# Kernel tuning notes

Measured on AMD Instinct MI355X. Metric: run time of the kernel, lower is better.

Reference implementation:

```python
import jax, jax.numpy as jnp
import numpy as np

N = 50000
E = 800000
IN, H1, H2, OUT = 128, 256, 256, 128


def gcn_conv(x, edge_index, W, b):
    """PyG GCNConv with normalize=True, add_self_loops=True.
    out = D^-1/2 (A + I) D^-1/2 (x @ W) + b, messages flow src->dst."""
    n = x.shape[0]
    h = x @ W  # [N, C_out]
    src, dst = edge_index[0], edge_index[1]
    # degree of (A + I) at each destination node (all edge weights = 1)
    deg = jax.ops.segment_sum(jnp.ones(src.shape[0], dtype=x.dtype), dst, num_segments=n) + 1.0
    dinv = jax.lax.rsqrt(deg)  # deg >= 1, safe
    norm = dinv[src] * dinv[dst]  # [E]
    agg = jax.ops.segment_sum(h[src] * norm[:, None], dst, num_segments=n)
    # self-loop contribution: norm_ii = dinv[i]^2
    return agg + h * (dinv * dinv)[:, None] + b


def setup_inputs() -> dict:
    key = jax.random.key(0)
    ks = jax.random.split(key, 12)
    node_feature = jax.random.normal(ks[0], (N, IN), dtype=jnp.float32)
    edge_index = jax.random.randint(ks[1], (2, E), 0, N, dtype=jnp.int64)
    edge_index_new = jax.random.randint(ks[2], (2, E), 0, N, dtype=jnp.int64)
    def glorot(k, fan_in, fan_out):
        s = jnp.sqrt(6.0 / (fan_in + fan_out)).astype(jnp.float32)
        return jax.random.uniform(k, (fan_in, fan_out), jnp.float32, -s, s)
    return {
        "node_feature": node_feature,
        "edge_index": edge_index,
        "edge_index_new": edge_index_new,
        "W0": glorot(ks[3], IN, H1), "b0": jnp.zeros((H1,), jnp.float32),
        "W1": glorot(ks[4], IN, H2), "b1": jnp.zeros((H2,), jnp.float32),
        "W2": glorot(ks[5], H1, OUT), "b2": jnp.zeros((OUT,), jnp.float32),
        "W3": glorot(ks[6], H2, OUT), "b3": jnp.zeros((OUT,), jnp.float32),
    }


def reference(node_feature, edge_index, edge_index_new, W0, b0, W1, b1, W2, b2, W3, b3):
    tmp1 = jax.nn.relu(gcn_conv(node_feature, edge_index, W0, b0))
    tmp2 = jax.nn.relu(gcn_conv(node_feature, edge_index_new, W1, b1))
    out1 = gcn_conv(tmp1, edge_index, W2, b2)
    out2 = gcn_conv(tmp2, edge_index_new, W3, b3)
    return out1 + out2
```

## Files before the change

kernel.cpp:

```cpp
#include <hip/hip_runtime.h>


typedef unsigned int uint;
typedef unsigned short ushort;
typedef __attribute__((ext_vector_type(8))) short bf8_t;
typedef __attribute__((ext_vector_type(4))) float f4_t;

#define CHUNK 4096
#define MAXNB 800

__device__ inline ushort f2bf(float f) {
    uint u = __float_as_uint(f);
    return (ushort)((u + 0x7fff + ((u >> 16) & 1)) >> 16);
}
__device__ inline float bf2f(ushort h) { return __uint_as_float(((uint)h) << 16); }

__global__ __launch_bounds__(256) void k_p1_hist(
    const int* __restrict__ ei_a, const int* __restrict__ ei_b,
    int* __restrict__ cnt_mat, int e, int NB, int NW) {
    __shared__ int lh[MAXNB];
    int l = blockIdx.x / NW, w = blockIdx.x % NW;
    const int* dst = (l ? ei_b : ei_a) + e;
    for (int t = threadIdx.x; t < NB; t += 256) lh[t] = 0;
    __syncthreads();
    int beg = w * CHUNK, end = min(beg + CHUNK, e);
    for (int j = beg + threadIdx.x; j < end; j += 256) atomicAdd(&lh[dst[j] >> 6], 1);
    __syncthreads();
    int* outp = cnt_mat + ((size_t)l * NW + w) * NB;
    for (int t = threadIdx.x; t < NB; t += 256) outp[t] = lh[t];
}

__global__ __launch_bounds__(256) void k_p2a(const int* __restrict__ cnt_mat,
                                             int* __restrict__ wgoff, int* __restrict__ btot,
                                             int NB, int NW) {
    __shared__ int s[256];
    int which = blockIdx.x;
    int l = which / NB, b = which - l * NB;
    int t = threadIdx.x;
    int v = (t < NW) ? cnt_mat[((size_t)l * NW + t) * NB + b] : 0;
    s[t] = v;
    __syncthreads();
    for (int o = 1; o < 256; o <<= 1) {
        int x = 0;
        if (t >= o) x = s[t - o];
        __syncthreads();
        s[t] += x;
        __syncthreads();
    }
    if (t < NW) wgoff[((size_t)l * NB + b) * NW + t] = s[t] - v;
    if (t == 255) btot[which] = s[255];
}

__global__ __launch_bounds__(256) void k_p2b(const int* __restrict__ btot,
                                             int* __restrict__ boff, int NB, int e) {
    __shared__ int s[1024];
    for (int l = 0; l < 2; ++l) {
        for (int t = threadIdx.x; t < 1024; t += 256) s[t] = (t < NB) ? btot[l * NB + t] : 0;
        __syncthreads();
        for (int o = 1; o < 1024; o <<= 1) {
            int tmp[4];
#pragma unroll
            for (int k = 0; k < 4; ++k) {
                int idx = threadIdx.x + k * 256;
                tmp[k] = (idx >= o) ? s[idx - o] : 0;
            }
            __syncthreads();
#pragma unroll
            for (int k = 0; k < 4; ++k) s[threadIdx.x + k * 256] += tmp[k];
            __syncthreads();
        }
        for (int t = threadIdx.x; t < NB; t += 256)
            boff[l * (NB + 1) + t] = s[t] - btot[l * NB + t];
        if (threadIdx.x == 0) boff[l * (NB + 1) + NB] = e;
        __syncthreads();
    }
}

__global__ __launch_bounds__(256) void k_p3_scatter(
    const int* __restrict__ ei_a, const int* __restrict__ ei_b,
    const int* __restrict__ wgoff, const int* __restrict__ boff,
    int* __restrict__ ebuf_a, int* __restrict__ ebuf_b, int e, int NB, int NW) {
    __shared__ int base[MAXNB];
    __shared__ int bump[MAXNB];
    int l = blockIdx.x / NW, w = blockIdx.x % NW;
    const int* ei = l ? ei_b : ei_a;
    int* ebuf = l ? ebuf_b : ebuf_a;
    for (int t = threadIdx.x; t < NB; t += 256) {
        base[t] = boff[l * (NB + 1) + t] + wgoff[((size_t)l * NB + t) * NW + w];
        bump[t] = 0;
    }
    __syncthreads();
    int beg = w * CHUNK, end = min(beg + CHUNK, e);
    for (int j = beg + threadIdx.x; j < end; j += 256) {
        int sv = ei[j], d = ei[e + j];
        int b = d >> 6;
        int pos = base[b] + atomicAdd(&bump[b], 1);
        ebuf[pos] = ((d & 63) << 17) | sv;
    }
}

__global__ __launch_bounds__(256) void k_p4_nodesort(
    const int* __restrict__ ebuf_a, const int* __restrict__ ebuf_b,
    const int* __restrict__ boff, int* __restrict__ csr_a, int* __restrict__ csr_b,
    int* __restrict__ noff, float* __restrict__ dinv, int n, int e, int NB) {
    __shared__ int hist[64], nstart[64];
    int which = blockIdx.x;
    int l = which / NB, b = which - l * NB;
    const int* ebuf = l ? ebuf_b : ebuf_a;
    int* csr = l ? csr_b : csr_a;
    int seg0 = boff[l * (NB + 1) + b], seg1 = boff[l * (NB + 1) + b + 1];
    if (threadIdx.x < 64) hist[threadIdx.x] = 0;
    __syncthreads();
    for (int j = seg0 + (int)threadIdx.x; j < seg1; j += 256)
        atomicAdd(&hist[ebuf[j] >> 17], 1);
    __syncthreads();
    if (threadIdx.x < 64) {
        int v = hist[threadIdx.x];
        int s = v;
#pragma unroll
        for (int o = 1; o < 64; o <<= 1) {
            int t = __shfl_up(s, o, 64);
            if ((int)threadIdx.x >= o) s += t;
        }
        int node = b * 64 + (int)threadIdx.x;
        nstart[threadIdx.x] = seg0 + s - v;
        if (node < n) {
            noff[(size_t)l * (n + 1) + node] = seg0 + s - v;
            dinv[(size_t)l * n + node] = rsqrtf((float)v + 1.0f);
        }
        hist[threadIdx.x] = 0;
    }
    if (b == NB - 1 && threadIdx.x == 0) noff[(size_t)l * (n + 1) + n] = e;
    __syncthreads();
    for (int j = seg0 + (int)threadIdx.x; j < seg1; j += 256) {
        int pk = ebuf[j];
        int ni = pk >> 17;
        int pos = nstart[ni] + atomicAdd(&hist[ni], 1);
        csr[pos] = pk & 0x1ffff;
    }
}

__global__ void k_cvt(const float2* __restrict__ x2, const float* __restrict__ dinv,
                      uint* __restrict__ xba, uint* __restrict__ xbb, int n) {
    int i = blockIdx.x * blockDim.x + threadIdx.x;
    if (i >= n * 64) return;
    int node = i >> 6;
    float da = dinv[node], db = dinv[n + node];
    float2 v = x2[i];
    xba[i] = (uint)f2bf(da * v.x) | ((uint)f2bf(da * v.y) << 16);
    xbb[i] = (uint)f2bf(db * v.x) | ((uint)f2bf(db * v.y) << 16);
}

__global__ void k_pack_all(const float* __restrict__ W0, const float* __restrict__ W1,
                           const float* __restrict__ W2, const float* __restrict__ W3,
                           ushort* __restrict__ Wpb) {
    int i = blockIdx.x * blockDim.x + threadIdx.x;
    if (i >= 4 * 32768) return;
    int seg = i >> 15;
    int r = i & 32767;
    const float* W = seg == 0 ? W0 : seg == 1 ? W1 : seg == 2 ? W2 : W3;
    int N = seg < 2 ? 256 : 128;
    int k = r / N, nn = r - k * N;
    int kt = k >> 5, q = (k & 31) >> 3, jj = k & 7;
    int nt = nn >> 4, ln = q * 16 + (nn & 15);
    int NT = N >> 4;
    Wpb[(size_t)seg * 32768 + (((size_t)(kt * NT + nt)) * 64 + ln) * 8 + jj] = f2bf(W[r]);
}

__device__ inline void gather_row(const uint* __restrict__ xb, const int* __restrict__ ep,
                                  int m, int lane, float& ax, float& ay) {
    int j = 0;
    for (; j + 8 <= m; j += 8) {
        int4 s4 = *(const int4*)(ep + j);
        int4 s5 = *(const int4*)(ep + j + 4);
        uint u0 = xb[(size_t)s4.x * 64 + lane];
        uint u1 = xb[(size_t)s4.y * 64 + lane];
        uint u2 = xb[(size_t)s4.z * 64 + lane];
        uint u3 = xb[(size_t)s4.w * 64 + lane];
        uint u4 = xb[(size_t)s5.x * 64 + lane];
        uint u5 = xb[(size_t)s5.y * 64 + lane];
        uint u6 = xb[(size_t)s5.z * 64 + lane];
        uint u7 = xb[(size_t)s5.w * 64 + lane];
        ax += bf2f((ushort)u0) + bf2f((ushort)u1) + bf2f((ushort)u2) + bf2f((ushort)u3) +
              bf2f((ushort)u4) + bf2f((ushort)u5) + bf2f((ushort)u6) + bf2f((ushort)u7);
        ay += bf2f((ushort)(u0 >> 16)) + bf2f((ushort)(u1 >> 16)) +
              bf2f((ushort)(u2 >> 16)) + bf2f((ushort)(u3 >> 16)) +
              bf2f((ushort)(u4 >> 16)) + bf2f((ushort)(u5 >> 16)) +
              bf2f((ushort)(u6 >> 16)) + bf2f((ushort)(u7 >> 16));
    }
    for (; j + 4 <= m; j += 4) {
        int4 s4 = *(const int4*)(ep + j);
        uint u0 = xb[(size_t)s4.x * 64 + lane];
        uint u1 = xb[(size_t)s4.y * 64 + lane];
        uint u2 = xb[(size_t)s4.z * 64 + lane];
        uint u3 = xb[(size_t)s4.w * 64 + lane];
        ax += bf2f((ushort)u0) + bf2f((ushort)u1) + bf2f((ushort)u2) + bf2f((ushort)u3);
        ay += bf2f((ushort)(u0 >> 16)) + bf2f((ushort)(u1 >> 16)) +
              bf2f((ushort)(u2 >> 16)) + bf2f((ushort)(u3 >> 16));
    }
    for (; j < m; ++j) {
        uint u = xb[(size_t)ep[j] * 64 + lane];
        ax += bf2f((ushort)u);
        ay += bf2f((ushort)(u >> 16));
    }
}

__global__ __launch_bounds__(256) void k_gather_l1(
    const uint* __restrict__ xba, const uint* __restrict__ xbb,
    const int* __restrict__ csr_a, const int* __restrict__ csr_b,
    const int* __restrict__ noff, const float* __restrict__ dinv,
    uint* __restrict__ ta, uint* __restrict__ tb, int n, int gb) {
    int bid = blockIdx.x;
    int br = bid >= gb;
    const uint* xb = br ? xbb : xba;
    const int* csr = br ? csr_b : csr_a;
    const int* no = noff + (size_t)br * (n + 1);
    const float* dv = dinv + (size_t)br * n;
    uint* outp = br ? tb : ta;
    int node = ((bid - (br ? gb : 0)) * 256 + (int)threadIdx.x) >> 6;
    if (node >= n) return;
    node = __builtin_amdgcn_readfirstlane(node);
    const int lane = threadIdx.x & 63;
    int beg = no[node], m = no[node + 1] - beg;
    uint us = xb[(size_t)node * 64 + lane];
    float ax = 0.f, ay = 0.f;
    gather_row(xb, csr + beg, m, lane, ax, ay);
    float di = dv[node];
    uint o = (uint)f2bf(di * (ax + bf2f((ushort)us))) |
             ((uint)f2bf(di * (ay + bf2f((ushort)(us >> 16)))) << 16);
    outp[(size_t)node * 64 + lane] = o;
}

__global__ __launch_bounds__(256) void k_gather_l2(
    const uint* __restrict__ hba, const uint* __restrict__ hbb,
    const int* __restrict__ csr_a, const int* __restrict__ csr_b,
    const int* __restrict__ noff, const float* __restrict__ dinv,
    const float* __restrict__ b2, const float* __restrict__ b3,
    float* __restrict__ out, int n) {
    int node = (blockIdx.x * 256 + (int)threadIdx.x) >> 6;
    if (node >= n) return;
    node = __builtin_amdgcn_readfirstlane(node);
    const int lane = threadIdx.x & 63;

    int beg = noff[node], m = noff[node + 1] - beg;
    float ax = 0.f, ay = 0.f;
    gather_row(hba, csr_a + beg, m, lane, ax, ay);
    uint usa = hba[(size_t)node * 64 + lane];
    float da = dinv[node];
    float vx = da * (ax + bf2f((ushort)usa));
    float vy = da * (ay + bf2f((ushort)(usa >> 16)));

    const int* no_b = noff + (n + 1);
    int beg2 = no_b[node], m2 = no_b[node + 1] - beg2;
    float bx = 0.f, by = 0.f;
    gather_row(hbb, csr_b + beg2, m2, lane, bx, by);
    uint usb = hbb[(size_t)node * 64 + lane];
    float db = dinv[n + node];
    vx += db * (bx + bf2f((ushort)usb));
    vy += db * (by + bf2f((ushort)(usb >> 16)));

    const int f = lane * 2;
    float2 o;
    o.x = b2[f] + b3[f] + vx;
    o.y = b2[f + 1] + b3[f + 1] + vy;
    *(float2*)(out + (size_t)node * 128 + f) = o;
}

__global__ __launch_bounds__(256) void k_mlp_fused(
    const ushort* __restrict__ ta, const ushort* __restrict__ tb,
    const ushort* __restrict__ Wpb, const float* __restrict__ b0,
    const float* __restrict__ b1, const float* __restrict__ dinv,
    ushort* __restrict__ oa, ushort* __restrict__ ob, int n) {
    constexpr int LDW = 264;
    __shared__ ushort hs[64 * LDW];
    const int br = blockIdx.y;
    const ushort* Ap  = br ? tb : ta;
    const ushort* W1  = Wpb + (br ? 32768 : 0);
    const ushort* W2  = Wpb + (br ? 3 * 32768 : 2 * 32768);
    const float* bias = br ? b1 : b0;
    const float* dv   = dinv + (br ? n : 0);
    ushort* Cout      = br ? ob : oa;

    const int lane = threadIdx.x & 63;
    const int wave = threadIdx.x >> 6;
    const int l15 = lane & 15;
    const int quad = lane >> 4;
    const int row_blk = blockIdx.x * 64;

    {
        f4_t acc[4][4];
#pragma unroll
        for (int a = 0; a < 4; ++a)
#pragma unroll
            for (int b = 0; b < 4; ++b) acc[a][b] = (f4_t){0.f, 0.f, 0.f, 0.f};

#pragma unroll
        for (int kt = 0; kt < 4; ++kt) {
            bf8_t af[4];
#pragma unroll
            for (int mi = 0; mi < 4; ++mi) {
                int row = row_blk + mi * 16 + l15;
                if (row < n)
                    af[mi] = *(const bf8_t*)(Ap + (size_t)row * 128 + kt * 32 + quad * 8);
                else
                    af[mi] = (bf8_t){0, 0, 0, 0, 0, 0, 0, 0};
            }
#pragma unroll
            for (int nj = 0; nj < 4; ++nj) {
                int nt = wave * 4 + nj;
                bf8_t wf = *(const bf8_t*)(W1 + (((size_t)(kt * 16 + nt)) * 64 + lane) * 8);
#pragma unroll
                for (int mi = 0; mi < 4; ++mi)
                    acc[mi][nj] = __builtin_amdgcn_mfma_f32_16x16x32_bf16(af[mi], wf, acc[mi][nj], 0, 0, 0);
            }
        }
#pragma unroll
        for (int nj = 0; nj < 4; ++nj) {
            int col = wave * 64 + nj * 16 + l15;
            float bv = bias[col];
#pragma unroll
            for (int mi = 0; mi < 4; ++mi)
#pragma unroll
                for (int r = 0; r < 4; ++r) {
                    int rl = mi * 16 + quad * 4 + r;
                    hs[rl * LDW + col] = f2bf(fmaxf(acc[mi][nj][r] + bv, 0.f));
                }
        }
    }
    __syncthreads();

    {
        f4_t acc2[4][2];
#pragma unroll
        for (int a = 0; a < 4; ++a)
#pragma unroll
            for (int b = 0; b < 2; ++b) acc2[a][b] = (f4_t){0.f, 0.f, 0.f, 0.f};

#pragma unroll
        for (int kt = 0; kt < 8; ++kt) {
            bf8_t af[4];
#pragma unroll
            for (int mi = 0; mi < 4; ++mi)
                af[mi] = *(const bf8_t*)&hs[(mi * 16 + l15) * LDW + kt * 32 + quad * 8];
#pragma unroll
            for (int nj = 0; nj < 2; ++nj) {
                int nt = wave * 2 + nj;
                bf8_t wf = *(const bf8_t*)(W2 + (((size_t)(kt * 8 + nt)) * 64 + lane) * 8);
#pragma unroll
                for (int mi = 0; mi < 4; ++mi)
                    acc2[mi][nj] = __builtin_amdgcn_mfma_f32_16x16x32_bf16(af[mi], wf, acc2[mi][nj], 0, 0, 0);
            }
        }
#pragma unroll
        for (int nj = 0; nj < 2; ++nj) {
            int col = wave * 32 + nj * 16 + l15;
#pragma unroll
            for (int mi = 0; mi < 4; ++mi)
#pragma unroll
                for (int r = 0; r < 4; ++r) {
                    int row = row_blk + mi * 16 + quad * 4 + r;
                    if (row < n)
                        Cout[(size_t)row * 128 + col] = f2bf(acc2[mi][nj][r] * dv[row]);
                }
        }
    }
}

extern "C" void kernel_launch(void* const* d_in, const int* in_sizes, int n_in,
                              void* d_out, int out_size, void* d_ws, size_t ws_size,
                              hipStream_t stream) {
    const float* x    = (const float*)d_in[0];
    const int*   ei_a = (const int*)d_in[1];
    const int*   ei_b = (const int*)d_in[2];
    const float* W0 = (const float*)d_in[3];
    const float* b0 = (const float*)d_in[4];
    const float* W1 = (const float*)d_in[5];
    const float* b1 = (const float*)d_in[6];
    const float* W2 = (const float*)d_in[7];
    const float* b2 = (const float*)d_in[8];
    const float* W3 = (const float*)d_in[9];
    const float* b3 = (const float*)d_in[10];
    float* out = (float*)d_out;

    const int n = in_sizes[0] / 128;
    const int e = in_sizes[1] / 2;
    const int NB = (n + 63) / 64;
    const int NW = (e + CHUNK - 1) / CHUNK;

    float*  ws    = (float*)d_ws;
    float*  dinv  = ws;
    uint*   ta    = (uint*)(ws + 2 * (size_t)n);
    uint*   tb    = ta + 64 * (size_t)n;
    uint*   xba   = tb + 64 * (size_t)n;
    uint*   xbb   = xba + 64 * (size_t)n;
    uint*   oa    = xbb + 64 * (size_t)n;
    uint*   ob    = oa + 64 * (size_t)n;
    ushort* Wpb   = (ushort*)(ob + 64 * (size_t)n);
    int* cnt_mat  = (int*)(Wpb + 4 * 32768);
    int* wgoff    = cnt_mat + 2 * (size_t)NW * NB;
    int* btot     = wgoff + 2 * (size_t)NB * NW;
    int* boff     = btot + 2 * NB;
    int* noff     = boff + 2 * (NB + 1);
    int* ebuf_a   = noff + 2 * (n + 1);
    int* ebuf_b   = ebuf_a + e;
    int* csr_a    = ebuf_b + e;
    int* csr_b    = csr_a + e;

    const int B = 256;

    k_p1_hist<<<2 * NW, B, 0, stream>>>(ei_a, ei_b, cnt_mat, e, NB, NW);
    k_p2a<<<2 * NB, B, 0, stream>>>(cnt_mat, wgoff, btot, NB, NW);
    k_p2b<<<1, B, 0, stream>>>(btot, boff, NB, e);
    k_p3_scatter<<<2 * NW, B, 0, stream>>>(ei_a, ei_b, wgoff, boff, ebuf_a, ebuf_b, e, NB, NW);
    k_p4_nodesort<<<2 * NB, B, 0, stream>>>(ebuf_a, ebuf_b, boff, csr_a, csr_b, noff, dinv,
                                            n, e, NB);

    k_cvt<<<(n * 64 + B - 1) / B, B, 0, stream>>>((const float2*)x, dinv, xba, xbb, n);
    k_pack_all<<<(4 * 32768 + B - 1) / B, B, 0, stream>>>(W0, W1, W2, W3, Wpb);

    const int gb = (n + 3) / 4;
    const int mblocks = (n + 63) / 64;

    k_gather_l1<<<2 * gb, B, 0, stream>>>(xba, xbb, csr_a, csr_b, noff, dinv, ta, tb, n, gb);

    k_mlp_fused<<<dim3(mblocks, 2), B, 0, stream>>>((const ushort*)ta, (const ushort*)tb,
                                                    Wpb, b0, b1, dinv,
                                                    (ushort*)oa, (ushort*)ob, n);

    k_gather_l2<<<gb, B, 0, stream>>>(oa, ob, csr_a, csr_b, noff, dinv, b2, b3, out, n);
}
```

Baseline: 314.5 us.

## Fuse layer-1 gather into MLP kernel, widen sort buckets, merge cvt/pack

Layer-1 neighbour aggregation now writes its 32-row tile straight into swizzled shared memory, and the two-layer MFMA MLP consumes it in the same kernel. This removes the global round trip of the aggregated intermediate and one launch. The edge sort now uses 256-node buckets instead of 64, so there are fewer buckets and less scan and scatter overhead, and the cvt and weight-pack kernels are merged into one launch. The trade-offs are a smaller MLP tile with lower MFMA reuse per block and gather latency now in the MLP's critical path. The 256-bucket sort also assumes NB is at most 256, which holds for n=50000.

```diff
diff --git a/kernel.cpp b/kernel.cpp
--- a/kernel.cpp
+++ b/kernel.cpp
@@ -7,7 +7,7 @@
 typedef __attribute__((ext_vector_type(4))) float f4_t;
 
 #define CHUNK 4096
-#define MAXNB 800
+#define BKT 256
 
 __device__ inline ushort f2bf(float f) {
     uint u = __float_as_uint(f);
@@ -18,16 +18,16 @@
 __global__ __launch_bounds__(256) void k_p1_hist(
     const int* __restrict__ ei_a, const int* __restrict__ ei_b,
     int* __restrict__ cnt_mat, int e, int NB, int NW) {
-    __shared__ int lh[MAXNB];
+    __shared__ int lh[BKT];
     int l = blockIdx.x / NW, w = blockIdx.x % NW;
     const int* dst = (l ? ei_b : ei_a) + e;
-    for (int t = threadIdx.x; t < NB; t += 256) lh[t] = 0;
+    if (threadIdx.x < NB) lh[threadIdx.x] = 0;
     __syncthreads();
     int beg = w * CHUNK, end = min(beg + CHUNK, e);
-    for (int j = beg + threadIdx.x; j < end; j += 256) atomicAdd(&lh[dst[j] >> 6], 1);
+    for (int j = beg + threadIdx.x; j < end; j += 256) atomicAdd(&lh[dst[j] >> 8], 1);
     __syncthreads();
     int* outp = cnt_mat + ((size_t)l * NW + w) * NB;
-    for (int t = threadIdx.x; t < NB; t += 256) outp[t] = lh[t];
+    if (threadIdx.x < NB) outp[threadIdx.x] = lh[threadIdx.x];
 }
 
 __global__ __launch_bounds__(256) void k_p2a(const int* __restrict__ cnt_mat,
@@ -53,25 +53,21 @@
 
 __global__ __launch_bounds__(256) void k_p2b(const int* __restrict__ btot,
                                              int* __restrict__ boff, int NB, int e) {
-    __shared__ int s[1024];
+    __shared__ int s[256];
     for (int l = 0; l < 2; ++l) {
-        for (int t = threadIdx.x; t < 1024; t += 256) s[t] = (t < NB) ? btot[l * NB + t] : 0;
-        __syncthreads();
-        for (int o = 1; o < 1024; o <<= 1) {
-            int tmp[4];
-#pragma unroll
-            for (int k = 0; k < 4; ++k) {
-                int idx = threadIdx.x + k * 256;
-                tmp[k] = (idx >= o) ? s[idx - o] : 0;
-            }
+        int t = threadIdx.x;
+        int v = (t < NB) ? btot[l * NB + t] : 0;
+        s[t] = v;
+        __syncthreads();
+        for (int o = 1; o < 256; o <<= 1) {
+            int x = 0;
+            if (t >= o) x = s[t - o];
             __syncthreads();
-#pragma unroll
-            for (int k = 0; k < 4; ++k) s[threadIdx.x + k * 256] += tmp[k];
+            s[t] += x;
             __syncthreads();
         }
-        for (int t = threadIdx.x; t < NB; t += 256)
-            boff[l * (NB + 1) + t] = s[t] - btot[l * NB + t];
-        if (threadIdx.x == 0) boff[l * (NB + 1) + NB] = e;
+        if (t < NB) boff[l * (NB + 1) + t] = s[t] - v;
+        if (t == 0) boff[l * (NB + 1) + NB] = e;
         __syncthreads();
     }
 }
@@ -80,22 +76,23 @@
     const int* __restrict__ ei_a, const int* __restrict__ ei_b,
     const int* __restrict__ wgoff, const int* __restrict__ boff,
     int* __restrict__ ebuf_a, int* __restrict__ ebuf_b, int e, int NB, int NW) {
-    __shared__ int base[MAXNB];
-    __shared__ int bump[MAXNB];
+    __shared__ int base[BKT];
+    __shared__ int bump[BKT];
     int l = blockIdx.x / NW, w = blockIdx.x % NW;
     const int* ei = l ? ei_b : ei_a;
     int* ebuf = l ? ebuf_b : ebuf_a;
-    for (int t = threadIdx.x; t < NB; t += 256) {
-        base[t] = boff[l * (NB + 1) + t] + wgoff[((size_t)l * NB + t) * NW + w];
-        bump[t] = 0;
+    if (threadIdx.x < NB) {
+        base[threadIdx.x] = boff[l * (NB + 1) + threadIdx.x] +
+                            wgoff[((size_t)l * NB + threadIdx.x) * NW + w];
+        bump[threadIdx.x] = 0;
     }
     __syncthreads();
     int beg = w * CHUNK, end = min(beg + CHUNK, e);
     for (int j = beg + threadIdx.x; j < end; j += 256) {
         int sv = ei[j], d = ei[e + j];
-        int b = d >> 6;
+        int b = d >> 8;
         int pos = base[b] + atomicAdd(&bump[b], 1);
-        ebuf[pos] = ((d & 63) << 17) | sv;
+        ebuf[pos] = ((d & 255) << 17) | sv;
     }
 }
 
@@ -103,36 +100,37 @@
     const int* __restrict__ ebuf_a, const int* __restrict__ ebuf_b,
     const int* __restrict__ boff, int* __restrict__ csr_a, int* __restrict__ csr_b,
     int* __restrict__ noff, float* __restrict__ dinv, int n, int e, int NB) {
-    __shared__ int hist[64], nstart[64];
+    __shared__ int hist[256], nstart[256], sc[256];
     int which = blockIdx.x;
     int l = which / NB, b = which - l * NB;
     const int* ebuf = l ? ebuf_b : ebuf_a;
     int* csr = l ? csr_b : csr_a;
     int seg0 = boff[l * (NB + 1) + b], seg1 = boff[l * (NB + 1) + b + 1];
-    if (threadIdx.x < 64) hist[threadIdx.x] = 0;
-    __syncthreads();
-    for (int j = seg0 + (int)threadIdx.x; j < seg1; j += 256)
-        atomicAdd(&hist[ebuf[j] >> 17], 1);
-    __syncthreads();
-    if (threadIdx.x < 64) {
-        int v = hist[threadIdx.x];
-        int s = v;
-#pragma unroll
-        for (int o = 1; o < 64; o <<= 1) {
-            int t = __shfl_up(s, o, 64);
-            if ((int)threadIdx.x >= o) s += t;
-        }
-        int node = b * 64 + (int)threadIdx.x;
-        nstart[threadIdx.x] = seg0 + s - v;
-        if (node < n) {
-            noff[(size_t)l * (n + 1) + node] = seg0 + s - v;
-            dinv[(size_t)l * n + node] = rsqrtf((float)v + 1.0f);
-        }
-        hist[threadIdx.x] = 0;
-    }
-    if (b == NB - 1 && threadIdx.x == 0) noff[(size_t)l * (n + 1) + n] = e;
-    __syncthreads();
-    for (int j = seg0 + (int)threadIdx.x; j < seg1; j += 256) {
+    int t = threadIdx.x;
+    hist[t] = 0;
+    __syncthreads();
+    for (int j = seg0 + t; j < seg1; j += 256) atomicAdd(&hist[ebuf[j] >> 17], 1);
+    __syncthreads();
+    int v = hist[t];
+    sc[t] = v;
+    __syncthreads();
+    for (int o = 1; o < 256; o <<= 1) {
+        int x = 0;
+        if (t >= o) x = sc[t - o];
+        __syncthreads();
+        sc[t] += x;
+        __syncthreads();
+    }
+    nstart[t] = seg0 + sc[t] - v;
+    int node = b * BKT + t;
+    if (node < n) {
+        noff[(size_t)l * (n + 1) + node] = nstart[t];
+        dinv[(size_t)l * n + node] = rsqrtf((float)v + 1.0f);
+    }
+    hist[t] = 0;
+    if (b == NB - 1 && t == 0) noff[(size_t)l * (n + 1) + n] = e;
+    __syncthreads();
+    for (int j = seg0 + t; j < seg1; j += 256) {
         int pk = ebuf[j];
         int ni = pk >> 17;
         int pos = nstart[ni] + atomicAdd(&hist[ni], 1);
@@ -140,31 +138,32 @@
     }
 }
 
-__global__ void k_cvt(const float2* __restrict__ x2, const float* __restrict__ dinv,
-                      uint* __restrict__ xba, uint* __restrict__ xbb, int n) {
-    int i = blockIdx.x * blockDim.x + threadIdx.x;
-    if (i >= n * 64) return;
-    int node = i >> 6;
-    float da = dinv[node], db = dinv[n + node];
-    float2 v = x2[i];
-    xba[i] = (uint)f2bf(da * v.x) | ((uint)f2bf(da * v.y) << 16);
-    xbb[i] = (uint)f2bf(db * v.x) | ((uint)f2bf(db * v.y) << 16);
-}
-
-__global__ void k_pack_all(const float* __restrict__ W0, const float* __restrict__ W1,
+__global__ void k_cvt_pack(const float2* __restrict__ x2, const float* __restrict__ dinv,
+                           uint* __restrict__ xba, uint* __restrict__ xbb,
+                           const float* __restrict__ W0, const float* __restrict__ W1,
                            const float* __restrict__ W2, const float* __restrict__ W3,
-                           ushort* __restrict__ Wpb) {
-    int i = blockIdx.x * blockDim.x + threadIdx.x;
-    if (i >= 4 * 32768) return;
-    int seg = i >> 15;
-    int r = i & 32767;
-    const float* W = seg == 0 ? W0 : seg == 1 ? W1 : seg == 2 ? W2 : W3;
-    int N = seg < 2 ? 256 : 128;
-    int k = r / N, nn = r - k * N;
-    int kt = k >> 5, q = (k & 31) >> 3, jj = k & 7;
-    int nt = nn >> 4, ln = q * 16 + (nn & 15);
-    int NT = N >> 4;
-    Wpb[(size_t)seg * 32768 + (((size_t)(kt * NT + nt)) * 64 + ln) * 8 + jj] = f2bf(W[r]);
+                           ushort* __restrict__ Wpb, int n, int cvtb) {
+    if ((int)blockIdx.x < cvtb) {
+        int i = blockIdx.x * 256 + threadIdx.x;
+        if (i >= n * 64) return;
+        int node = i >> 6;
+        float da = dinv[node], db = dinv[n + node];
+        float2 v = x2[i];
+        xba[i] = (uint)f2bf(da * v.x) | ((uint)f2bf(da * v.y) << 16);
+        xbb[i] = (uint)f2bf(db * v.x) | ((uint)f2bf(db * v.y) << 16);
+    } else {
+        int i = (blockIdx.x - cvtb) * 256 + threadIdx.x;
+        if (i >= 4 * 32768) return;
+        int seg = i >> 15;
+        int r = i & 32767;
+        const float* W = seg == 0 ? W0 : seg == 1 ? W1 : seg == 2 ? W2 : W3;
+        int N = seg < 2 ? 256 : 128;
+        int k = r / N, nn = r - k * N;
+        int kt = k >> 5, q = (k & 31) >> 3, jj = k & 7;
+        int nt = nn >> 4, ln = q * 16 + (nn & 15);
+        int NT = N >> 4;
+        Wpb[(size_t)seg * 32768 + (((size_t)(kt * NT + nt)) * 64 + ln) * 8 + jj] = f2bf(W[r]);
+    }
 }
 
 __device__ inline void gather_row(const uint* __restrict__ xb, const int* __restrict__ ep,
@@ -205,30 +204,127 @@
     }
 }
 
-__global__ __launch_bounds__(256) void k_gather_l1(
+__global__ __launch_bounds__(256) void k_gather_mlp(
     const uint* __restrict__ xba, const uint* __restrict__ xbb,
     const int* __restrict__ csr_a, const int* __restrict__ csr_b,
     const int* __restrict__ noff, const float* __restrict__ dinv,
-    uint* __restrict__ ta, uint* __restrict__ tb, int n, int gb) {
+    const ushort* __restrict__ Wpb, const float* __restrict__ b0,
+    const float* __restrict__ b1, ushort* __restrict__ oa, ushort* __restrict__ ob,
+    int n, int nblk) {
+    constexpr int HW = 264;
+    __shared__ uint As32[32 * 64];
+    __shared__ ushort hs[32 * HW];
+
     int bid = blockIdx.x;
-    int br = bid >= gb;
+    int br = bid >= nblk;
+    int blk = br ? bid - nblk : bid;
     const uint* xb = br ? xbb : xba;
     const int* csr = br ? csr_b : csr_a;
     const int* no = noff + (size_t)br * (n + 1);
     const float* dv = dinv + (size_t)br * n;
-    uint* outp = br ? tb : ta;
-    int node = ((bid - (br ? gb : 0)) * 256 + (int)threadIdx.x) >> 6;
-    if (node >= n) return;
-    node = __builtin_amdgcn_readfirstlane(node);
+    const ushort* W1 = Wpb + (br ? 32768 : 0);
+    const ushort* W2 = Wpb + (br ? 3 * 32768 : 2 * 32768);
+    const float* bias = br ? b1 : b0;
+    ushort* Cout = br ? ob : oa;
+
     const int lane = threadIdx.x & 63;
-    int beg = no[node], m = no[node + 1] - beg;
-    uint us = xb[(size_t)node * 64 + lane];
-    float ax = 0.f, ay = 0.f;
-    gather_row(xb, csr + beg, m, lane, ax, ay);
-    float di = dv[node];
-    uint o = (uint)f2bf(di * (ax + bf2f((ushort)us))) |
-             ((uint)f2bf(di * (ay + bf2f((ushort)(us >> 16)))) << 16);
-    outp[(size_t)node * 64 + lane] = o;
+    const int wave = threadIdx.x >> 6;
+    const int l15 = lane & 15;
+    const int quad = lane >> 4;
+    const int row0 = blk * 32;
+
+    for (int k = 0; k < 8; ++k) {
+        int r = wave * 8 + k;
+        int node = row0 + r;
+        uint o = 0;
+        if (node < n) {
+            node = __builtin_amdgcn_readfirstlane(node);
+            int beg = no[node], m = no[node + 1] - beg;
+            float ax = 0.f, ay = 0.f;
+            gather_row(xb, csr + beg, m, lane, ax, ay);
+            uint us = xb[(size_t)node * 64 + lane];
+            float di = dv[node];
+            o = (uint)f2bf(di * (ax + bf2f((ushort)us))) |
+                ((uint)f2bf(di * (ay + bf2f((ushort)(us >> 16)))) << 16);
+        }
+        int dw = ((((lane >> 2) + r) & 15) << 2) | (lane & 3);
+        As32[r * 64 + dw] = o;
+    }
+    __syncthreads();
+
+    {
+        f4_t acc[2][4];
+#pragma unroll
+        for (int a = 0; a < 2; ++a)
+#pragma unroll
+            for (int b = 0; b < 4; ++b) acc[a][b] = (f4_t){0.f, 0.f, 0.f, 0.f};
+
+#pragma unroll
+        for (int kt = 0; kt < 4; ++kt) {
+            bf8_t af[2];
+#pragma unroll
+            for (int mi = 0; mi < 2; ++mi) {
+                int rr = mi * 16 + l15;
+                int blk16 = (kt * 4 + quad + rr) & 15;
+                af[mi] = *(const bf8_t*)&As32[rr * 64 + blk16 * 4];
+            }
+#pragma unroll
+            for (int nj = 0; nj < 4; ++nj) {
+                int nt = wave * 4 + nj;
+                bf8_t wf = *(const bf8_t*)(W1 + (((size_t)(kt * 16 + nt)) * 64 + lane) * 8);
+#pragma unroll
+                for (int mi = 0; mi < 2; ++mi)
+                    acc[mi][nj] = __builtin_amdgcn_mfma_f32_16x16x32_bf16(af[mi], wf, acc[mi][nj], 0, 0, 0);
+            }
+        }
+#pragma unroll
+        for (int nj = 0; nj < 4; ++nj) {
+            int col = wave * 64 + nj * 16 + l15;
+            float bv = bias[col];
+#pragma unroll
+            for (int mi = 0; mi < 2; ++mi)
+#pragma unroll
+                for (int r = 0; r < 4; ++r)
+                    hs[(mi * 16 + quad * 4 + r) * HW + col] = f2bf(fmaxf(acc[mi][nj][r] + bv, 0.f));
+        }
+    }
+    __syncthreads();
+
+    {
+        f4_t acc2[2][2];
+#pragma unroll
+        for (int a = 0; a < 2; ++a)
+#pragma unroll
+            for (int b = 0; b < 2; ++b) acc2[a][b] = (f4_t){0.f, 0.f, 0.f, 0.f};
+
+#pragma unroll
+        for (int kt = 0; kt < 8; ++kt) {
+            bf8_t af[2];
+#pragma unroll
+            for (int mi = 0; mi < 2; ++mi)
+                af[mi] = *(const bf8_t*)&hs[(mi * 16 + l15) * HW + kt * 32 + quad * 8];
+#pragma unroll
+            for (int nj = 0; nj < 2; ++nj) {
+                int nt = wave * 2 + nj;
+                bf8_t wf = *(const bf8_t*)(W2 + (((size_t)(kt * 8 + nt)) * 64 + lane) * 8);
+#pragma unroll
+                for (int mi = 0; mi < 2; ++mi)
+                    acc2[mi][nj] = __builtin_amdgcn_mfma_f32_16x16x32_bf16(af[mi], wf, acc2[mi][nj], 0, 0, 0);
+            }
+        }
+#pragma unroll
+        for (int nj = 0; nj < 2; ++nj) {
+            int col = wave * 32 + nj * 16 + l15;
+#pragma unroll
+            for (int mi = 0; mi < 2; ++mi)
+#pragma unroll
+                for (int r = 0; r < 4; ++r) {
+                    int row = row0 + mi * 16 + quad * 4 + r;
+                    if (row < n)
+                        Cout[(size_t)row * 128 + col] = f2bf(acc2[mi][nj][r] * dv[row]);
+                }
+        }
+    }
 }
 
 __global__ __launch_bounds__(256) void k_gather_l2(
@@ -264,106 +360,6 @@
     o.x = b2[f] + b3[f] + vx;
     o.y = b2[f + 1] + b3[f + 1] + vy;
     *(float2*)(out + (size_t)node * 128 + f) = o;
-}
-
-__global__ __launch_bounds__(256) void k_mlp_fused(
-    const ushort* __restrict__ ta, const ushort* __restrict__ tb,
-    const ushort* __restrict__ Wpb, const float* __restrict__ b0,
-    const float* __restrict__ b1, const float* __restrict__ dinv,
-    ushort* __restrict__ oa, ushort* __restrict__ ob, int n) {
-    constexpr int LDW = 264;
-    __shared__ ushort hs[64 * LDW];
-    const int br = blockIdx.y;
-    const ushort* Ap  = br ? tb : ta;
-    const ushort* W1  = Wpb + (br ? 32768 : 0);
-    const ushort* W2  = Wpb + (br ? 3 * 32768 : 2 * 32768);
-    const float* bias = br ? b1 : b0;
-    const float* dv   = dinv + (br ? n : 0);
-    ushort* Cout      = br ? ob : oa;
-
-    const int lane = threadIdx.x & 63;
-    const int wave = threadIdx.x >> 6;
-    const int l15 = lane & 15;
-    const int quad = lane >> 4;
-    const int row_blk = blockIdx.x * 64;
-
-    {
-        f4_t acc[4][4];
-#pragma unroll
-        for (int a = 0; a < 4; ++a)
-#pragma unroll
-            for (int b = 0; b < 4; ++b) acc[a][b] = (f4_t){0.f, 0.f, 0.f, 0.f};
-
-#pragma unroll
-        for (int kt = 0; kt < 4; ++kt) {
-            bf8_t af[4];
-#pragma unroll
-            for (int mi = 0; mi < 4; ++mi) {
-                int row = row_blk + mi * 16 + l15;
-                if (row < n)
-                    af[mi] = *(const bf8_t*)(Ap + (size_t)row * 128 + kt * 32 + quad * 8);
-                else
-                    af[mi] = (bf8_t){0, 0, 0, 0, 0, 0, 0, 0};
-            }
-#pragma unroll
-            for (int nj = 0; nj < 4; ++nj) {
-                int nt = wave * 4 + nj;
-                bf8_t wf = *(const bf8_t*)(W1 + (((size_t)(kt * 16 + nt)) * 64 + lane) * 8);
-#pragma unroll
-                for (int mi = 0; mi < 4; ++mi)
-                    acc[mi][nj] = __builtin_amdgcn_mfma_f32_16x16x32_bf16(af[mi], wf, acc[mi][nj], 0, 0, 0);
-            }
-        }
-#pragma unroll
-        for (int nj = 0; nj < 4; ++nj) {
-            int col = wave * 64 + nj * 16 + l15;
-            float bv = bias[col];
-#pragma unroll
-            for (int mi = 0; mi < 4; ++mi)
-#pragma unroll
-                for (int r = 0; r < 4; ++r) {
-                    int rl = mi * 16 + quad * 4 + r;
-                    hs[rl * LDW + col] = f2bf(fmaxf(acc[mi][nj][r] + bv, 0.f));
-                }
-        }
-    }
-    __syncthreads();
-
-    {
-        f4_t acc2[4][2];
-#pragma unroll
-        for (int a = 0; a < 4; ++a)
-#pragma unroll
-            for (int b = 0; b < 2; ++b) acc2[a][b] = (f4_t){0.f, 0.f, 0.f, 0.f};
-
-#pragma unroll
-        for (int kt = 0; kt < 8; ++kt) {
-            bf8_t af[4];
-#pragma unroll
-            for (int mi = 0; mi < 4; ++mi)
-                af[mi] = *(const bf8_t*)&hs[(mi * 16 + l15) * LDW + kt * 32 + quad * 8];
-#pragma unroll
-            for (int nj = 0; nj < 2; ++nj) {
-                int nt = wave * 2 + nj;
-                bf8_t wf = *(const bf8_t*)(W2 + (((size_t)(kt * 8 + nt)) * 64 + lane) * 8);
-#pragma unroll
-                for (int mi = 0; mi < 4; ++mi)
-                    acc2[mi][nj] = __builtin_amdgcn_mfma_f32_16x16x32_bf16(af[mi], wf, acc2[mi][nj], 0, 0, 0);
-            }
-        }
-#pragma unroll
-        for (int nj = 0; nj < 2; ++nj) {
-            int col = wave * 32 + nj * 16 + l15;
-#pragma unroll
-            for (int mi = 0; mi < 4; ++mi)
-#pragma unroll
-                for (int r = 0; r < 4; ++r) {
-                    int row = row_blk + mi * 16 + quad * 4 + r;
-                    if (row < n)
-                        Cout[(size_t)row * 128 + col] = f2bf(acc2[mi][nj][r] * dv[row]);
-                }
-        }
-    }
 }
 
 extern "C" void kernel_launch(void* const* d_in, const int* in_sizes, int n_in,
@@ -384,27 +380,25 @@
 
     const int n = in_sizes[0] / 128;
     const int e = in_sizes[1] / 2;
-    const int NB = (n + 63) / 64;
+    const int NB = (n + BKT - 1) / BKT;
     const int NW = (e + CHUNK - 1) / CHUNK;
 
-    float*  ws    = (float*)d_ws;
-    float*  dinv  = ws;
-    uint*   ta    = (uint*)(ws + 2 * (size_t)n);
-    uint*   tb    = ta + 64 * (size_t)n;
-    uint*   xba   = tb + 64 * (size_t)n;
-    uint*   xbb   = xba + 64 * (size_t)n;
-    uint*   oa    = xbb + 64 * (size_t)n;
-    uint*   ob    = oa + 64 * (size_t)n;
-    ushort* Wpb   = (ushort*)(ob + 64 * (size_t)n);
-    int* cnt_mat  = (int*)(Wpb + 4 * 32768);
-    int* wgoff    = cnt_mat + 2 * (size_t)NW * NB;
-    int* btot     = wgoff + 2 * (size_t)NB * NW;
-    int* boff     = btot + 2 * NB;
-    int* noff     = boff + 2 * (NB + 1);
-    int* ebuf_a   = noff + 2 * (n + 1);
-    int* ebuf_b   = ebuf_a + e;
-    int* csr_a    = ebuf_b + e;
-    int* csr_b    = csr_a + e;
+    float*  ws   = (float*)d_ws;
+    float*  dinv = ws;
+    uint*   xba  = (uint*)(ws + 2 * (size_t)n);
+    uint*   xbb  = xba + 64 * (size_t)n;
+    uint*   oa   = xbb + 64 * (size_t)n;
+    uint*   ob   = oa + 64 * (size_t)n;
+    ushort* Wpb  = (ushort*)(ob + 64 * (size_t)n);
+    int* cnt_mat = (int*)(Wpb + 4 * 32768);
+    int* wgoff   = cnt_mat + 2 * (size_t)NW * NB;
+    int* btot    = wgoff + 2 * (size_t)NB * NW;
+    int* boff    = btot + 2 * NB;
+    int* noff    = boff + 2 * (NB + 1);
+    int* ebuf_a  = noff + 2 * (n + 1);
+    int* ebuf_b  = ebuf_a + e;
+    int* csr_a   = ebuf_b + e;
+    int* csr_b   = csr_a + e;
 
     const int B = 256;
 
@@ -415,17 +409,15 @@
     k_p4_nodesort<<<2 * NB, B, 0, stream>>>(ebuf_a, ebuf_b, boff, csr_a, csr_b, noff, dinv,
                                             n, e, NB);
 
-    k_cvt<<<(n * 64 + B - 1) / B, B, 0, stream>>>((const float2*)x, dinv, xba, xbb, n);
-    k_pack_all<<<(4 * 32768 + B - 1) / B, B, 0, stream>>>(W0, W1, W2, W3, Wpb);
+    const int cvtb = (n * 64 + B - 1) / B;
+    const int packb = (4 * 32768 + B - 1) / B;
+    k_cvt_pack<<<cvtb + packb, B, 0, stream>>>((const float2*)x, dinv, xba, xbb,
+                                               W0, W1, W2, W3, Wpb, n, cvtb);
+
+    const int nblk = (n + 31) / 32;
+    k_gather_mlp<<<2 * nblk, B, 0, stream>>>(xba, xbb, csr_a, csr_b, noff, dinv, Wpb,
+                                             b0, b1, (ushort*)oa, (ushort*)ob, n, nblk);
 
     const int gb = (n + 3) / 4;
-    const int mblocks = (n + 63) / 64;
-
-    k_gather_l1<<<2 * gb, B, 0, stream>>>(xba, xbb, csr_a, csr_b, noff, dinv, ta, tb, n, gb);
-
-    k_mlp_fused<<<dim3(mblocks, 2), B, 0, stream>>>((const ushort*)ta, (const ushort*)tb,
-                                                    Wpb, b0, b1, dinv,
-                                                    (ushort*)oa, (ushort*)ob, n);
-
     k_gather_l2<<<gb, B, 0, stream>>>(oa, ob, csr_a, csr_b, noff, dinv, b2, b3, out, n);
 }
```

Measured after the change: 289.8 us. 1.09x faster.
